# Kernel tuning notes

Measured on AMD Instinct MI355X. Metric: run time of the kernel, lower is better.

## Reference

```python
import jax, jax.numpy as jnp
import numpy as np

B, T, D = 512, 128, 768
CD, SD, P = 192, 128, 128
FEAT = CD + SD + 1  # 321
LN_EPS = 1e-5


def setup_inputs() -> dict:
    key = jax.random.key(0)
    ks = jax.random.split(key, 10)
    return {
        'H': jax.random.normal(ks[0], (B, T, D), jnp.float32),
        'tt': jax.random.randint(ks[1], (B, T), 0, 2, jnp.int64),
        'attn': jnp.ones((B, T), jnp.int64),
        'Wc': jax.random.normal(ks[2], (CD, 2 * D), jnp.float32) * 0.02,
        'bc': jax.random.normal(ks[3], (CD,), jnp.float32) * 0.02,
        'Ws': jax.random.normal(ks[4], (SD, 2 * D), jnp.float32) * 0.02,
        'bs': jax.random.normal(ks[5], (SD,), jnp.float32) * 0.02,
        'gate': jnp.array([0.5], jnp.float32),
        'ln_g': jnp.ones((FEAT,), jnp.float32),
        'ln_b': jnp.zeros((FEAT,), jnp.float32),
        'Wcls': jax.random.normal(ks[6], (2, FEAT), jnp.float32) * 0.02,
        'bcls': jax.random.normal(ks[7], (2,), jnp.float32) * 0.02,
        'dirs': jax.random.normal(ks[8], (P, D), jnp.float32),
    }


def reference(H, tt, attn, Wc, bc, Ws, bs, gate, ln_g, ln_b, Wcls, bcls, dirs):
    dt = H.dtype
    cls = H[:, 0]                                   # [B, D]
    mask0 = (tt == 0) & (attn == 1)                 # [B, T]
    mask1 = (tt == 1) & (attn == 1)

    def mmean(mask):
        mf = mask.astype(dt)
        s = jnp.einsum('btd,bt->bd', H, mf)
        cnt = jnp.maximum(mask.sum(1, keepdims=True), 1).astype(dt)
        return s / cnt

    rep = jnp.concatenate([cls, mmean(mask0) - mmean(mask1)], axis=1)  # [B, 2D]
    C = rep @ Wc.T + bc
    S = rep @ Ws.T + bs
    g = jax.nn.sigmoid(gate)                        # [1]
    fused = jnp.concatenate([C * (1 - g), S * g], axis=1)  # [B, CD+SD]

    # batched max-sliced W1: project, push masked tokens to +inf, sort along T
    dirs_n = dirs / jnp.linalg.norm(dirs, axis=1, keepdims=True)
    proj = jnp.einsum('btd,pd->btp', H, dirs_n)     # [B, T, P]
    inf = jnp.asarray(jnp.inf, dt)
    xp = jnp.sort(jnp.where(mask0[:, :, None], proj, inf), axis=1)
    yp = jnp.sort(jnp.where(mask1[:, :, None], proj, inf), axis=1)
    n0 = mask0.sum(1)
    n1 = mask1.sum(1)
    mm = jnp.minimum(n0, n1)                        # [B] ragged truncation length
    valid = (jnp.arange(T)[None, :] < mm[:, None])[:, :, None]  # [B, T, 1]
    xs = jnp.where(valid, xp, 0.0)
    ys = jnp.where(valid, yp, 0.0)
    diff = jnp.abs(xs - ys).sum(1) / jnp.maximum(mm, 1)[:, None].astype(dt)  # [B, P]
    d_ot = diff.max(1, keepdims=True)               # [B, 1]

    feat = jnp.concatenate([fused, d_ot], axis=1)   # [B, 321]
    mu = feat.mean(-1, keepdims=True)
    var = feat.var(-1, keepdims=True)
    normed = (feat - mu) / jnp.sqrt(var + LN_EPS) * ln_g + ln_b
    logits = normed @ Wcls.T + bcls                 # [B, 2]

    ortho = jnp.mean((Wc @ Ws.T) ** 2)
    return logits, ortho
```

## Files before the change

### kernel.cpp

```cpp
#include <hip/hip_runtime.h>
#include <hip/hip_bf16.h>

constexpr int B_ = 512;
constexpr int T_ = 128;
constexpr int D_ = 768;
constexpr int CD_ = 192;
constexpr int SD_ = 128;
constexpr int P_ = 128;
constexpr int FEAT_ = 321;
constexpr float LN_EPS_ = 1e-5f;

constexpr size_t REP_SZ   = (size_t)B_ * 2 * D_;
constexpr size_t DN16_FLT = (size_t)P_ * D_ / 2;

typedef __attribute__((ext_vector_type(8))) short short8;
typedef __attribute__((ext_vector_type(4))) float f32x4;
typedef unsigned long long ull_t;

__device__ __forceinline__ unsigned short f2bf(float x) {
    unsigned u = __float_as_uint(x);
    return (unsigned short)((u + 0x7FFFu + ((u >> 16) & 1u)) >> 16);
}
__device__ __forceinline__ float bf2f(unsigned short h) {
    return __uint_as_float((unsigned)h << 16);
}

__global__ __launch_bounds__(256) void k_dirs(const float* __restrict__ dirs,
                                              unsigned short* __restrict__ dn16) {
    int p = blockIdx.x;
    int tid = threadIdx.x;
    float s = 0.f;
    for (int d = tid; d < D_; d += 256) {
        float v = dirs[(size_t)p * D_ + d];
        s = fmaf(v, v, s);
    }
    __shared__ float red[256];
    red[tid] = s;
    __syncthreads();
    for (int off = 128; off > 0; off >>= 1) {
        if (tid < off) red[tid] += red[tid + off];
        __syncthreads();
    }
    float inv = 1.0f / sqrtf(red[0]);
    for (int d = tid; d < D_; d += 256) {
        dn16[(size_t)p * D_ + d] = f2bf(dirs[(size_t)p * D_ + d] * inv);
    }
}

constexpr int NIT_ = 24;
constexpr int BUF_U16_ = 8192;

__global__ __launch_bounds__(512) void k_projsort(const float* __restrict__ H,
                                                  const int* __restrict__ tt,
                                                  const int* __restrict__ attn,
                                                  const unsigned short* __restrict__ dn16,
                                                  float* __restrict__ rep,
                                                  float* __restrict__ d_ot) {
    const int b = blockIdx.x;
    const int tid = threadIdx.x;
    const int lane = tid & 63;
    const int w = tid >> 6;
    const int wr = w >> 2;
    const int wc = w & 3;
    const int fr = lane & 15;
    const int kg = lane >> 4;

    __shared__ __align__(16) unsigned short stage[2 * BUF_U16_];
    __shared__ unsigned char xb[8192];
    __shared__ unsigned char yb[8192];
    __shared__ float dred[512];
    __shared__ unsigned short mask16[256];
    unsigned short* proj16 = stage;
    ull_t* xch = (ull_t*)dred;

    const float* Hb = H + (size_t)b * T_ * D_;
    const int srow = tid >> 2;
    const int scp  = tid & 3;
    const int sclog = scp ^ ((srow >> 1) & 3);
    const float* gA = Hb + (size_t)srow * D_ + sclog * 8;
    const unsigned short* gB = dn16 + (size_t)srow * D_ + sclog * 8;
    const int dOffA = srow * 32 + scp * 8;
    const int dOffB = 4096 + dOffA;

    float4 a0A = *reinterpret_cast<const float4*>(gA);
    float4 a1A = *reinterpret_cast<const float4*>(gA + 4);
    short8 bvA = *reinterpret_cast<const short8*>(gB);
    float4 a0B = *reinterpret_cast<const float4*>(gA + 32);
    float4 a1B = *reinterpret_cast<const float4*>(gA + 36);
    short8 bvB = *reinterpret_cast<const short8*>(gB + 32);

    const int myt = 64 * wr + lane;
    int vt = tt[b * T_ + myt];
    int va = attn[b * T_ + myt];
    bool m0 = (vt == 0) && (va == 1);
    bool m1 = (vt == 1) && (va == 1);
    ull_t bal0 = __ballot(m0);
    ull_t bal1 = __ballot(m1);
    if (lane == 0 && (w == 0 || w == 4)) {
        xch[wr * 2] = bal0;
        xch[wr * 2 + 1] = bal1;
    }
    if (tid < 128) {
        int t2 = tt[b * T_ + tid];
        int a2 = attn[b * T_ + tid];
        mask16[tid]       = (t2 == 0 && a2 == 1) ? 0x3F80u : 0u;
        mask16[128 + tid] = (t2 == 1 && a2 == 1) ? 0x3F80u : 0u;
    }
    __syncthreads();
    const ull_t lo0 = xch[0], lo1 = xch[1], hi0 = xch[2], hi1 = xch[3];
    const int n0 = __popcll(lo0) + __popcll(hi0);
    const int n1 = __popcll(lo1) + __popcll(hi1);
    const int ntot = n0 + n1;
    const float inv0 = 1.f / (float)max(n0, 1);
    const float inv1 = 1.f / (float)max(n1, 1);
    ull_t below = (1ull << lane) - 1ull;
    int mypos = 0xFF;
    if (m0) mypos = (wr ? __popcll(lo0) : 0) + __popcll((wr ? hi0 : lo0) & below);
    else if (m1) mypos = n0 + (wr ? __popcll(lo1) : 0) + __popcll((wr ? hi1 : lo1) & below);
    __syncthreads();

    const int ck = (kg ^ ((fr >> 1) & 3)) * 8;
    const int baseA = (64 * wr + fr) * 32 + ck;
    const int baseB = 4096 + (32 * wc + fr) * 32 + ck;
    const int grp = w & 1;
    const int dl = grp * 16 + fr;
    const int dch = dl >> 3, dsub = dl & 7;
    float* repb = rep + (size_t)b * 2 * D_;

    f32x4 acc[4][2];
#pragma unroll
    for (int m = 0; m < 4; ++m)
#pragma unroll
        for (int n = 0; n < 2; ++n) acc[m][n] = (f32x4){0.f, 0.f, 0.f, 0.f};

    auto body = [&](int it, unsigned short* sb, float4& pa0, float4& pa1, short8& pbv) {
        short8 wv;
        wv[0] = (short)f2bf(pa0.x); wv[1] = (short)f2bf(pa0.y);
        wv[2] = (short)f2bf(pa0.z); wv[3] = (short)f2bf(pa0.w);
        wv[4] = (short)f2bf(pa1.x); wv[5] = (short)f2bf(pa1.y);
        wv[6] = (short)f2bf(pa1.z); wv[7] = (short)f2bf(pa1.w);
        *reinterpret_cast<short8*>(sb + dOffA) = wv;
        *reinterpret_cast<short8*>(sb + dOffB) = pbv;
        if (srow == 0) {
            float* cd = repb + it * 32 + sclog * 8;
            *reinterpret_cast<float4*>(cd)     = pa0;
            *reinterpret_cast<float4*>(cd + 4) = pa1;
        }
        if (it + 2 < NIT_) {
            int k = (it + 2) * 32;
            pa0 = *reinterpret_cast<const float4*>(gA + k);
            pa1 = *reinterpret_cast<const float4*>(gA + k + 4);
            pbv = *reinterpret_cast<const short8*>(gB + k);
        }
        asm volatile("s_waitcnt lgkmcnt(0)" ::: "memory");
        __builtin_amdgcn_s_barrier();
        asm volatile("" ::: "memory");

        short8 af[4], bf_[2];
#pragma unroll
        for (int m = 0; m < 4; ++m)
            af[m] = *reinterpret_cast<const short8*>(sb + baseA + 512 * m);
#pragma unroll
        for (int n = 0; n < 2; ++n)
            bf_[n] = *reinterpret_cast<const short8*>(sb + baseB + 512 * n);
#pragma unroll
        for (int m = 0; m < 4; ++m)
#pragma unroll
            for (int n = 0; n < 2; ++n)
                acc[m][n] = __builtin_amdgcn_mfma_f32_16x16x32_bf16(af[m], bf_[n], acc[m][n], 0, 0, 0);

        bool duty = ((it & 1) == 0) ? (w == 0 || w == 1) : (w == 4 || w == 5);
        if (duty) {
            f32x4 ar = (f32x4){0.f, 0.f, 0.f, 0.f};
#pragma unroll
            for (int tc = 0; tc < 4; ++tc) {
                int tbase = tc * 32 + kg * 8;
                short8 am = {0, 0, 0, 0, 0, 0, 0, 0};
                if (fr < 2) am = *reinterpret_cast<const short8*>(&mask16[fr * 128 + tbase]);
                short8 bm;
#pragma unroll
                for (int j = 0; j < 8; ++j) {
                    int t = tbase + j;
                    bm[j] = (short)sb[t * 32 + (dch ^ ((t >> 1) & 3)) * 8 + dsub];
                }
                ar = __builtin_amdgcn_mfma_f32_16x16x32_bf16(am, bm, ar, 0, 0, 0);
            }
            if (lane < 16)
                repb[D_ + it * 32 + grp * 16 + lane] = ar[0] * inv0 - ar[1] * inv1;
        }
        asm volatile("" ::: "memory");
        __builtin_amdgcn_s_barrier();
        asm volatile("" ::: "memory");
    };

    for (int mi = 0; mi < NIT_ / 2; ++mi) {
        body(2 * mi,     stage,            a0A, a1A, bvA);
        body(2 * mi + 1, stage + BUF_U16_, a0B, a1B, bvB);
    }
    __syncthreads();

#pragma unroll
    for (int m = 0; m < 4; ++m) {
#pragma unroll
        for (int r = 0; r < 4; ++r) {
            int rowlane = 16 * m + kg * 4 + r;
            int pp = __shfl(mypos, rowlane);
            if (pp != 0xFF) {
#pragma unroll
                for (int n = 0; n < 2; ++n) {
                    int col = 32 * wc + 16 * n + fr;
                    unsigned bb = f2bf(acc[m][n][r]);
                    unsigned su = bb ^ ((bb >> 15) ? 0xFFFFu : 0x8000u);
                    proj16[pp * 128 + col] = (unsigned short)su;
                }
            }
        }
    }
    __syncthreads();

    const int mmv = min(n0, n1);
    const int c = tid & 127;
    const int q = tid >> 7;
#pragma unroll
    for (int pass = 0; pass < 2; ++pass) {
        const int pbase = q * 32 + pass * 16;
        unsigned kv[16];
        int cnt[16];
#pragma unroll
        for (int ii = 0; ii < 16; ++ii) {
            int p = pbase + ii;
            unsigned key = 0xFFFFFFFFu;
            if (p < ntot) {
                unsigned su = proj16[p * 128 + c];
                key = ((unsigned)(p >= n0) << 31) | (su << 8) | (unsigned)p;
            }
            kv[ii] = key;
            cnt[ii] = 0;
        }
        int lo, hi;
        if (pbase + 16 <= n0) { lo = 0;  hi = n0;   }
        else if (pbase >= n0) { lo = n0; hi = ntot; }
        else                  { lo = 0;  hi = ntot; }
        for (int j = lo; j < hi; ++j) {
            unsigned su = proj16[j * 128 + c];
            unsigned kw = ((unsigned)(j >= n0) << 31) | (su << 8) | (unsigned)j;
#pragma unroll
            for (int ii = 0; ii < 16; ++ii) cnt[ii] += (kw < kv[ii]) ? 1 : 0;
        }
#pragma unroll
        for (int ii = 0; ii < 16; ++ii) {
            int p = pbase + ii;
            if (p < ntot) {
                int rank = cnt[ii] - ((p >= n0 && lo == 0) ? n0 : 0);
                if (rank < mmv) {
                    unsigned char* buf = (p >= n0) ? yb : xb;
                    buf[rank * 128 + c] = (unsigned char)p;
                }
            }
        }
    }
    __syncthreads();

    float part = 0.f;
    for (int r = q; r < mmv; r += 4) {
        unsigned sx = proj16[(int)xb[r * 128 + c] * 128 + c];
        unsigned sy = proj16[(int)yb[r * 128 + c] * 128 + c];
        unsigned bx = sx ^ ((sx >> 15) ? 0x8000u : 0xFFFFu);
        unsigned byv = sy ^ ((sy >> 15) ? 0x8000u : 0xFFFFu);
        part += fabsf(bf2f((unsigned short)bx) - bf2f((unsigned short)byv));
    }
    dred[tid] = part;
    __syncthreads();
    if (tid < 128) {
        float invm = 1.f / (float)max(mmv, 1);
        dred[tid] = (dred[tid] + dred[tid + 128] + dred[tid + 256] + dred[tid + 384]) * invm;
    }
    __syncthreads();
    if (tid < 64) {
        float m = fmaxf(dred[tid], dred[tid + 64]);
#pragma unroll
        for (int off = 32; off > 0; off >>= 1) m = fmaxf(m, __shfl_xor(m, off));
        if (tid == 0) d_ot[b] = m;
    }
}

__global__ __launch_bounds__(320) void k_head(const float* __restrict__ rep,
                                              const float* __restrict__ Wc,
                                              const float* __restrict__ bc,
                                              const float* __restrict__ Ws,
                                              const float* __restrict__ bs,
                                              const float* __restrict__ gate,
                                              const float* __restrict__ lng,
                                              const float* __restrict__ lnb,
                                              const float* __restrict__ Wcls,
                                              const float* __restrict__ bcls,
                                              const float* __restrict__ d_ot,
                                              float* __restrict__ out) {
    int b0 = blockIdx.x * 4;
    int tid = threadIdx.x;
    __shared__ __align__(16) float repS[4 * 1536];
    __shared__ float featS[4 * FEAT_];

    const float4* repg = reinterpret_cast<const float4*>(rep + (size_t)b0 * 1536);
    float4* repl = reinterpret_cast<float4*>(repS);
    for (int i = tid; i < 1536; i += 320) repl[i] = repg[i];
    __syncthreads();

    float g = 1.f / (1.f + expf(-gate[0]));

    {
        int o = tid;
        bool isC = o < CD_;
        const float* wptr = isC ? (Wc + (size_t)o * 1536) : (Ws + (size_t)(o - CD_) * 1536);
        float bias = isC ? bc[o] : bs[o - CD_];
        float scale = isC ? (1.f - g) : g;
        const float4* w4 = reinterpret_cast<const float4*>(wptr);
        float a0 = 0.f, a1 = 0.f, a2 = 0.f, a3 = 0.f;
        for (int k4 = 0; k4 < 384; ++k4) {
            float4 wv = w4[k4];
            float4 r0 = repl[k4];
            float4 r1 = repl[384 + k4];
            float4 r2 = repl[768 + k4];
            float4 r3 = repl[1152 + k4];
            a0 += fmaf(wv.x, r0.x, fmaf(wv.y, r0.y, fmaf(wv.z, r0.z, wv.w * r0.w)));
            a1 += fmaf(wv.x, r1.x, fmaf(wv.y, r1.y, fmaf(wv.z, r1.z, wv.w * r1.w)));
            a2 += fmaf(wv.x, r2.x, fmaf(wv.y, r2.y, fmaf(wv.z, r2.z, wv.w * r2.w)));
            a3 += fmaf(wv.x, r3.x, fmaf(wv.y, r3.y, fmaf(wv.z, r3.z, wv.w * r3.w)));
        }
        featS[0 * FEAT_ + o] = (a0 + bias) * scale;
        featS[1 * FEAT_ + o] = (a1 + bias) * scale;
        featS[2 * FEAT_ + o] = (a2 + bias) * scale;
        featS[3 * FEAT_ + o] = (a3 + bias) * scale;
    }
    if (tid < 4) featS[tid * FEAT_ + 320] = d_ot[b0 + tid];
    __syncthreads();

    int w = tid >> 6, lane = tid & 63;
    if (w < 4) {
        const float* f = featS + w * FEAT_;
        float s = 0.f, s2 = 0.f;
        for (int i = lane; i < FEAT_; i += 64) {
            float v = f[i];
            s += v;
            s2 = fmaf(v, v, s2);
        }
#pragma unroll
        for (int off = 32; off > 0; off >>= 1) {
            s += __shfl_xor(s, off);
            s2 += __shfl_xor(s2, off);
        }
        float mu = s * (1.f / (float)FEAT_);
        float var = fmaxf(s2 * (1.f / (float)FEAT_) - mu * mu, 0.f);
        float rstd = 1.0f / sqrtf(var + LN_EPS_);
        float l0 = 0.f, l1 = 0.f;
        for (int i = lane; i < FEAT_; i += 64) {
            float nv = (f[i] - mu) * rstd * lng[i] + lnb[i];
            l0 = fmaf(nv, Wcls[i], l0);
            l1 = fmaf(nv, Wcls[FEAT_ + i], l1);
        }
#pragma unroll
        for (int off = 32; off > 0; off >>= 1) {
            l0 += __shfl_xor(l0, off);
            l1 += __shfl_xor(l1, off);
        }
        if (lane == 0) {
            out[(size_t)(b0 + w) * 2 + 0] = l0 + bcls[0];
            out[(size_t)(b0 + w) * 2 + 1] = l1 + bcls[1];
        }
    }
}

__global__ __launch_bounds__(256) void k_ortho(const float* __restrict__ Wc,
                                               const float* __restrict__ Ws,
                                               float* __restrict__ part) {
    int i = blockIdx.x;
    int tid = threadIdx.x;
    __shared__ float wrow[1536];
    __shared__ float tmp[256];
    for (int k = tid; k < 1536; k += 256) wrow[k] = Wc[(size_t)i * 1536 + k];
    __syncthreads();
    int j = tid & 127, h = tid >> 7;
    const float* wsr = Ws + (size_t)j * 1536 + h * 768;
    const float* wr = wrow + h * 768;
    float s = 0.f;
    for (int k = 0; k < 768; ++k) s = fmaf(wr[k], wsr[k], s);
    tmp[tid] = s;
    __syncthreads();
    if (tid < 128) {
        float d = tmp[tid] + tmp[tid + 128];
        tmp[tid] = d * d;
    }
    __syncthreads();
    for (int off = 64; off > 0; off >>= 1) {
        if (tid < off) tmp[tid] += tmp[tid + off];
        __syncthreads();
    }
    if (tid == 0) part[i] = tmp[0];
}

__global__ __launch_bounds__(256) void k_ortho2(const float* __restrict__ part,
                                                float* __restrict__ out) {
    int tid = threadIdx.x;
    __shared__ float red[256];
    red[tid] = (tid < CD_) ? part[tid] : 0.f;
    __syncthreads();
    for (int off = 128; off > 0; off >>= 1) {
        if (tid < off) red[tid] += red[tid + off];
        __syncthreads();
    }
    if (tid == 0) out[(size_t)B_ * 2] = red[0] / (float)(CD_ * SD_);
}

extern "C" void kernel_launch(void* const* d_in, const int* in_sizes, int n_in,
                              void* d_out, int out_size, void* d_ws, size_t ws_size,
                              hipStream_t stream) {
    const float* H    = (const float*)d_in[0];
    const int*   tt   = (const int*)d_in[1];
    const int*   attn = (const int*)d_in[2];
    const float* Wc   = (const float*)d_in[3];
    const float* bc   = (const float*)d_in[4];
    const float* Ws   = (const float*)d_in[5];
    const float* bs   = (const float*)d_in[6];
    const float* gate = (const float*)d_in[7];
    const float* lng  = (const float*)d_in[8];
    const float* lnb  = (const float*)d_in[9];
    const float* Wcls = (const float*)d_in[10];
    const float* bcls = (const float*)d_in[11];
    const float* dirs = (const float*)d_in[12];

    float* ws    = (float*)d_ws;
    float* rep   = ws;
    unsigned short* dn16 = (unsigned short*)(ws + REP_SZ);
    float* dot   = ws + REP_SZ + DN16_FLT;
    float* part  = dot + B_;
    float* out   = (float*)d_out;

    k_dirs<<<P_, 256, 0, stream>>>(dirs, dn16);
    k_projsort<<<B_, 512, 0, stream>>>(H, tt, attn, dn16, rep, dot);
    k_head<<<B_ / 4, 320, 0, stream>>>(rep, Wc, bc, Ws, bs, gate, lng, lnb, Wcls, bcls, dot, out);
    k_ortho<<<CD_, 256, 0, stream>>>(Wc, Ws, part);
    k_ortho2<<<1, 256, 0, stream>>>(part, out);
}
```

Before: 187.6 us.

## Widen projection K-step to 64, single staging buffer, merge ortho into prologue/head

```diff
diff --git a/kernel.cpp b/kernel.cpp
--- a/kernel.cpp
+++ b/kernel.cpp
@@ -25,30 +25,57 @@
     return __uint_as_float((unsigned)h << 16);
 }
 
-__global__ __launch_bounds__(256) void k_dirs(const float* __restrict__ dirs,
-                                              unsigned short* __restrict__ dn16) {
-    int p = blockIdx.x;
+__global__ __launch_bounds__(256) void k_pre(const float* __restrict__ dirs,
+                                             const float* __restrict__ Wc,
+                                             const float* __restrict__ Ws,
+                                             unsigned short* __restrict__ dn16,
+                                             float* __restrict__ part) {
     int tid = threadIdx.x;
-    float s = 0.f;
-    for (int d = tid; d < D_; d += 256) {
-        float v = dirs[(size_t)p * D_ + d];
-        s = fmaf(v, v, s);
-    }
-    __shared__ float red[256];
-    red[tid] = s;
-    __syncthreads();
-    for (int off = 128; off > 0; off >>= 1) {
-        if (tid < off) red[tid] += red[tid + off];
-        __syncthreads();
-    }
-    float inv = 1.0f / sqrtf(red[0]);
-    for (int d = tid; d < D_; d += 256) {
-        dn16[(size_t)p * D_ + d] = f2bf(dirs[(size_t)p * D_ + d] * inv);
-    }
-}
-
-constexpr int NIT_ = 24;
-constexpr int BUF_U16_ = 8192;
+    if (blockIdx.x < 128) {
+        int p = blockIdx.x;
+        float s = 0.f;
+        for (int d = tid; d < D_; d += 256) {
+            float v = dirs[(size_t)p * D_ + d];
+            s = fmaf(v, v, s);
+        }
+        __shared__ float red[256];
+        red[tid] = s;
+        __syncthreads();
+        for (int off = 128; off > 0; off >>= 1) {
+            if (tid < off) red[tid] += red[tid + off];
+            __syncthreads();
+        }
+        float inv = 1.0f / sqrtf(red[0]);
+        for (int d = tid; d < D_; d += 256) {
+            dn16[(size_t)p * D_ + d] = f2bf(dirs[(size_t)p * D_ + d] * inv);
+        }
+    } else {
+        int i = blockIdx.x - 128;
+        __shared__ float wrow[1536];
+        __shared__ float tmp[256];
+        for (int k = tid; k < 1536; k += 256) wrow[k] = Wc[(size_t)i * 1536 + k];
+        __syncthreads();
+        int j = tid & 127, h = tid >> 7;
+        const float* wsr = Ws + (size_t)j * 1536 + h * 768;
+        const float* wr = wrow + h * 768;
+        float s = 0.f;
+        for (int k = 0; k < 768; ++k) s = fmaf(wr[k], wsr[k], s);
+        tmp[tid] = s;
+        __syncthreads();
+        if (tid < 128) {
+            float d = tmp[tid] + tmp[tid + 128];
+            tmp[tid] = d * d;
+        }
+        __syncthreads();
+        for (int off = 64; off > 0; off >>= 1) {
+            if (tid < off) tmp[tid] += tmp[tid + off];
+            __syncthreads();
+        }
+        if (tid == 0) part[i] = tmp[0];
+    }
+}
+
+constexpr int NIT_ = 12;
 
 __global__ __launch_bounds__(512) void k_projsort(const float* __restrict__ H,
                                                   const int* __restrict__ tt,
@@ -65,7 +92,7 @@
     const int fr = lane & 15;
     const int kg = lane >> 4;
 
-    __shared__ __align__(16) unsigned short stage[2 * BUF_U16_];
+    __shared__ __align__(16) unsigned short stage[16384];
     __shared__ unsigned char xb[8192];
     __shared__ unsigned char yb[8192];
     __shared__ float dred[512];
@@ -75,19 +102,33 @@
 
     const float* Hb = H + (size_t)b * T_ * D_;
     const int srow = tid >> 2;
-    const int scp  = tid & 3;
-    const int sclog = scp ^ ((srow >> 1) & 3);
-    const float* gA = Hb + (size_t)srow * D_ + sclog * 8;
-    const unsigned short* gB = dn16 + (size_t)srow * D_ + sclog * 8;
-    const int dOffA = srow * 32 + scp * 8;
-    const int dOffB = 4096 + dOffA;
-
-    float4 a0A = *reinterpret_cast<const float4*>(gA);
-    float4 a1A = *reinterpret_cast<const float4*>(gA + 4);
-    short8 bvA = *reinterpret_cast<const short8*>(gB);
-    float4 a0B = *reinterpret_cast<const float4*>(gA + 32);
-    float4 a1B = *reinterpret_cast<const float4*>(gA + 36);
-    short8 bvB = *reinterpret_cast<const short8*>(gB + 32);
+    const int c4   = tid & 3;
+    const int swz  = (srow >> 1) & 7;
+    const int p0c  = c4;
+    const int p1c  = c4 + 4;
+    const int l0c  = p0c ^ swz;
+    const int l1c  = p1c ^ swz;
+    const float* gA0 = Hb + (size_t)srow * D_ + l0c * 8;
+    const float* gA1 = Hb + (size_t)srow * D_ + l1c * 8;
+    const unsigned short* gB0 = dn16 + (size_t)srow * D_ + l0c * 8;
+    const unsigned short* gB1 = dn16 + (size_t)srow * D_ + l1c * 8;
+    const int wOffA0 = srow * 64 + p0c * 8;
+    const int wOffA1 = srow * 64 + p1c * 8;
+    const int wOffB0 = 8192 + wOffA0;
+    const int wOffB1 = 8192 + wOffA1;
+
+    float4 x0A = *reinterpret_cast<const float4*>(gA0);
+    float4 x1A = *reinterpret_cast<const float4*>(gA0 + 4);
+    float4 x2A = *reinterpret_cast<const float4*>(gA1);
+    float4 x3A = *reinterpret_cast<const float4*>(gA1 + 4);
+    short8 v0A = *reinterpret_cast<const short8*>(gB0);
+    short8 v1A = *reinterpret_cast<const short8*>(gB1);
+    float4 x0B = *reinterpret_cast<const float4*>(gA0 + 64);
+    float4 x1B = *reinterpret_cast<const float4*>(gA0 + 68);
+    float4 x2B = *reinterpret_cast<const float4*>(gA1 + 64);
+    float4 x3B = *reinterpret_cast<const float4*>(gA1 + 68);
+    short8 v0B = *reinterpret_cast<const short8*>(gB0 + 64);
+    short8 v1B = *reinterpret_cast<const short8*>(gB1 + 64);
 
     const int myt = 64 * wr + lane;
     int vt = tt[b * T_ + myt];
@@ -119,12 +160,22 @@
     else if (m1) mypos = n0 + (wr ? __popcll(lo1) : 0) + __popcll((wr ? hi1 : lo1) & below);
     __syncthreads();
 
-    const int ck = (kg ^ ((fr >> 1) & 3)) * 8;
-    const int baseA = (64 * wr + fr) * 32 + ck;
-    const int baseB = 4096 + (32 * wc + fr) * 32 + ck;
+    int addrA[4], addrB[2];
+#pragma unroll
+    for (int m = 0; m < 4; ++m) {
+        int row = 64 * wr + 16 * m + fr;
+        addrA[m] = row * 64 + (kg ^ ((row >> 1) & 7)) * 8;
+    }
+#pragma unroll
+    for (int n = 0; n < 2; ++n) {
+        int row = 32 * wc + 16 * n + fr;
+        addrB[n] = 8192 + row * 64 + (kg ^ ((row >> 1) & 7)) * 8;
+    }
+    const bool duty = (w == 0 || w == 1 || w == 4 || w == 5);
+    const int kcr = w >> 2;
     const int grp = w & 1;
-    const int dl = grp * 16 + fr;
-    const int dch = dl >> 3, dsub = dl & 7;
+    const int dk = kcr * 32 + grp * 16 + fr;
+    const int glc = dk >> 3, gsub = dk & 7;
     float* repb = rep + (size_t)b * 2 * D_;
 
     f32x4 acc[4][2];
@@ -133,43 +184,70 @@
 #pragma unroll
         for (int n = 0; n < 2; ++n) acc[m][n] = (f32x4){0.f, 0.f, 0.f, 0.f};
 
-    auto body = [&](int it, unsigned short* sb, float4& pa0, float4& pa1, short8& pbv) {
-        short8 wv;
-        wv[0] = (short)f2bf(pa0.x); wv[1] = (short)f2bf(pa0.y);
-        wv[2] = (short)f2bf(pa0.z); wv[3] = (short)f2bf(pa0.w);
-        wv[4] = (short)f2bf(pa1.x); wv[5] = (short)f2bf(pa1.y);
-        wv[6] = (short)f2bf(pa1.z); wv[7] = (short)f2bf(pa1.w);
-        *reinterpret_cast<short8*>(sb + dOffA) = wv;
-        *reinterpret_cast<short8*>(sb + dOffB) = pbv;
+    auto body = [&](int it, float4& pa0, float4& pa1, float4& pa2, float4& pa3,
+                    short8& pb0, short8& pb1) {
+        short8 wv0, wv1;
+        wv0[0] = (short)f2bf(pa0.x); wv0[1] = (short)f2bf(pa0.y);
+        wv0[2] = (short)f2bf(pa0.z); wv0[3] = (short)f2bf(pa0.w);
+        wv0[4] = (short)f2bf(pa1.x); wv0[5] = (short)f2bf(pa1.y);
+        wv0[6] = (short)f2bf(pa1.z); wv0[7] = (short)f2bf(pa1.w);
+        wv1[0] = (short)f2bf(pa2.x); wv1[1] = (short)f2bf(pa2.y);
+        wv1[2] = (short)f2bf(pa2.z); wv1[3] = (short)f2bf(pa2.w);
+        wv1[4] = (short)f2bf(pa3.x); wv1[5] = (short)f2bf(pa3.y);
+        wv1[6] = (short)f2bf(pa3.z); wv1[7] = (short)f2bf(pa3.w);
+        *reinterpret_cast<short8*>(&stage[wOffA0]) = wv0;
+        *reinterpret_cast<short8*>(&stage[wOffA1]) = wv1;
+        *reinterpret_cast<short8*>(&stage[wOffB0]) = pb0;
+        *reinterpret_cast<short8*>(&stage[wOffB1]) = pb1;
         if (srow == 0) {
-            float* cd = repb + it * 32 + sclog * 8;
-            *reinterpret_cast<float4*>(cd)     = pa0;
-            *reinterpret_cast<float4*>(cd + 4) = pa1;
+            float* cd = repb + it * 64;
+            *reinterpret_cast<float4*>(cd + l0c * 8)     = pa0;
+            *reinterpret_cast<float4*>(cd + l0c * 8 + 4) = pa1;
+            *reinterpret_cast<float4*>(cd + l1c * 8)     = pa2;
+            *reinterpret_cast<float4*>(cd + l1c * 8 + 4) = pa3;
         }
         if (it + 2 < NIT_) {
-            int k = (it + 2) * 32;
-            pa0 = *reinterpret_cast<const float4*>(gA + k);
-            pa1 = *reinterpret_cast<const float4*>(gA + k + 4);
-            pbv = *reinterpret_cast<const short8*>(gB + k);
+            int k = (it + 2) * 64;
+            pa0 = *reinterpret_cast<const float4*>(gA0 + k);
+            pa1 = *reinterpret_cast<const float4*>(gA0 + k + 4);
+            pa2 = *reinterpret_cast<const float4*>(gA1 + k);
+            pa3 = *reinterpret_cast<const float4*>(gA1 + k + 4);
+            pb0 = *reinterpret_cast<const short8*>(gB0 + k);
+            pb1 = *reinterpret_cast<const short8*>(gB1 + k);
         }
         asm volatile("s_waitcnt lgkmcnt(0)" ::: "memory");
         __builtin_amdgcn_s_barrier();
         asm volatile("" ::: "memory");
 
-        short8 af[4], bf_[2];
-#pragma unroll
-        for (int m = 0; m < 4; ++m)
-            af[m] = *reinterpret_cast<const short8*>(sb + baseA + 512 * m);
-#pragma unroll
-        for (int n = 0; n < 2; ++n)
-            bf_[n] = *reinterpret_cast<const short8*>(sb + baseB + 512 * n);
-#pragma unroll
-        for (int m = 0; m < 4; ++m)
+        {
+            short8 af[4], bf_[2];
+#pragma unroll
+            for (int m = 0; m < 4; ++m)
+                af[m] = *reinterpret_cast<const short8*>(&stage[addrA[m]]);
 #pragma unroll
             for (int n = 0; n < 2; ++n)
-                acc[m][n] = __builtin_amdgcn_mfma_f32_16x16x32_bf16(af[m], bf_[n], acc[m][n], 0, 0, 0);
-
-        bool duty = ((it & 1) == 0) ? (w == 0 || w == 1) : (w == 4 || w == 5);
+                bf_[n] = *reinterpret_cast<const short8*>(&stage[addrB[n]]);
+#pragma unroll
+            for (int m = 0; m < 4; ++m)
+#pragma unroll
+                for (int n = 0; n < 2; ++n)
+                    acc[m][n] = __builtin_amdgcn_mfma_f32_16x16x32_bf16(af[m], bf_[n], acc[m][n], 0, 0, 0);
+        }
+        {
+            short8 af[4], bf_[2];
+#pragma unroll
+            for (int m = 0; m < 4; ++m)
+                af[m] = *reinterpret_cast<const short8*>(&stage[addrA[m] ^ 32]);
+#pragma unroll
+            for (int n = 0; n < 2; ++n)
+                bf_[n] = *reinterpret_cast<const short8*>(&stage[addrB[n] ^ 32]);
+#pragma unroll
+            for (int m = 0; m < 4; ++m)
+#pragma unroll
+                for (int n = 0; n < 2; ++n)
+                    acc[m][n] = __builtin_amdgcn_mfma_f32_16x16x32_bf16(af[m], bf_[n], acc[m][n], 0, 0, 0);
+        }
+
         if (duty) {
             f32x4 ar = (f32x4){0.f, 0.f, 0.f, 0.f};
 #pragma unroll
@@ -181,12 +259,12 @@
 #pragma unroll
                 for (int j = 0; j < 8; ++j) {
                     int t = tbase + j;
-                    bm[j] = (short)sb[t * 32 + (dch ^ ((t >> 1) & 3)) * 8 + dsub];
+                    bm[j] = (short)stage[t * 64 + (glc ^ ((t >> 1) & 7)) * 8 + gsub];
                 }
                 ar = __builtin_amdgcn_mfma_f32_16x16x32_bf16(am, bm, ar, 0, 0, 0);
             }
             if (lane < 16)
-                repb[D_ + it * 32 + grp * 16 + lane] = ar[0] * inv0 - ar[1] * inv1;
+                repb[D_ + it * 64 + dk] = ar[0] * inv0 - ar[1] * inv1;
         }
         asm volatile("" ::: "memory");
         __builtin_amdgcn_s_barrier();
@@ -194,8 +272,8 @@
     };
 
     for (int mi = 0; mi < NIT_ / 2; ++mi) {
-        body(2 * mi,     stage,            a0A, a1A, bvA);
-        body(2 * mi + 1, stage + BUF_U16_, a0B, a1B, bvB);
+        body(2 * mi,     x0A, x1A, x2A, x3A, v0A, v1A);
+        body(2 * mi + 1, x0B, x1B, x2B, x3B, v0B, v1B);
     }
     __syncthreads();
 
@@ -295,11 +373,13 @@
                                               const float* __restrict__ Wcls,
                                               const float* __restrict__ bcls,
                                               const float* __restrict__ d_ot,
+                                              const float* __restrict__ part,
                                               float* __restrict__ out) {
     int b0 = blockIdx.x * 4;
     int tid = threadIdx.x;
     __shared__ __align__(16) float repS[4 * 1536];
     __shared__ float featS[4 * FEAT_];
+    __shared__ float ored[256];
 
     const float4* repg = reinterpret_cast<const float4*>(rep + (size_t)b0 * 1536);
     float4* repl = reinterpret_cast<float4*>(repS);
@@ -368,47 +448,21 @@
             out[(size_t)(b0 + w) * 2 + 1] = l1 + bcls[1];
         }
     }
-}
-
-__global__ __launch_bounds__(256) void k_ortho(const float* __restrict__ Wc,
-                                               const float* __restrict__ Ws,
-                                               float* __restrict__ part) {
-    int i = blockIdx.x;
-    int tid = threadIdx.x;
-    __shared__ float wrow[1536];
-    __shared__ float tmp[256];
-    for (int k = tid; k < 1536; k += 256) wrow[k] = Wc[(size_t)i * 1536 + k];
-    __syncthreads();
-    int j = tid & 127, h = tid >> 7;
-    const float* wsr = Ws + (size_t)j * 1536 + h * 768;
-    const float* wr = wrow + h * 768;
-    float s = 0.f;
-    for (int k = 0; k < 768; ++k) s = fmaf(wr[k], wsr[k], s);
-    tmp[tid] = s;
-    __syncthreads();
-    if (tid < 128) {
-        float d = tmp[tid] + tmp[tid + 128];
-        tmp[tid] = d * d;
-    }
-    __syncthreads();
-    for (int off = 64; off > 0; off >>= 1) {
-        if (tid < off) tmp[tid] += tmp[tid + off];
-        __syncthreads();
-    }
-    if (tid == 0) part[i] = tmp[0];
-}
-
-__global__ __launch_bounds__(256) void k_ortho2(const float* __restrict__ part,
-                                                float* __restrict__ out) {
-    int tid = threadIdx.x;
-    __shared__ float red[256];
-    red[tid] = (tid < CD_) ? part[tid] : 0.f;
-    __syncthreads();
-    for (int off = 128; off > 0; off >>= 1) {
-        if (tid < off) red[tid] += red[tid + off];
-        __syncthreads();
-    }
-    if (tid == 0) out[(size_t)B_ * 2] = red[0] / (float)(CD_ * SD_);
+
+    if (blockIdx.x == 0) {
+        __syncthreads();
+        if (tid < 256) {
+            ored[tid] = (tid < CD_) ? part[tid] : 0.f;
+        }
+        __syncthreads();
+        if (tid < 256) {
+            for (int off = 128; off > 0; off >>= 1) {
+                if (tid < off) ored[tid] += ored[tid + off];
+                __syncthreads();
+            }
+            if (tid == 0) out[(size_t)B_ * 2] = ored[0] / (float)(CD_ * SD_);
+        }
+    }
 }
 
 extern "C" void kernel_launch(void* const* d_in, const int* in_sizes, int n_in,
@@ -435,9 +489,7 @@
     float* part  = dot + B_;
     float* out   = (float*)d_out;
 
-    k_dirs<<<P_, 256, 0, stream>>>(dirs, dn16);
+    k_pre<<<320, 256, 0, stream>>>(dirs, Wc, Ws, dn16, part);
     k_projsort<<<B_, 512, 0, stream>>>(H, tt, attn, dn16, rep, dot);
-    k_head<<<B_ / 4, 320, 0, stream>>>(rep, Wc, bc, Ws, bs, gate, lng, lnb, Wcls, bcls, dot, out);
-    k_ortho<<<CD_, 256, 0, stream>>>(Wc, Ws, part);
-    k_ortho2<<<1, 256, 0, stream>>>(part, out);
-}
+    k_head<<<B_ / 4, 320, 0, stream>>>(rep, Wc, bc, Ws, bs, gate, lng, lnb, Wcls, bcls, dot, part, out);
+}
```

After: 206.2 us. +9.9%, slower.
